# Kernel tuning notes

Measured on AMD Instinct MI355X. Metric: run time of the kernel, lower is better.

The kernel has to match this reference:

```python
import jax, jax.numpy as jnp
import numpy as np

BN_EPS = 1e-5


def setup_inputs() -> dict:
    key = jax.random.key(0)
    ks = jax.random.split(key, 8)
    B, C, H, W = 8, 256, 64, 64
    Ci = 128
    x = jax.random.normal(ks[0], (B, C, H, W), dtype=jnp.float32)
    # 1x1 conv weights stored as [out, in] (kernel size 1 squeezed)
    sc = 1.0 / np.sqrt(C)
    g_w = jax.random.uniform(ks[1], (Ci, C), jnp.float32, -sc, sc)
    g_b = jax.random.uniform(ks[2], (Ci,), jnp.float32, -sc, sc)
    theta_w = jax.random.uniform(ks[3], (Ci, C), jnp.float32, -sc, sc)
    theta_b = jax.random.uniform(ks[4], (Ci,), jnp.float32, -sc, sc)
    phi_w = jax.random.uniform(ks[5], (Ci, C), jnp.float32, -sc, sc)
    phi_b = jax.random.uniform(ks[6], (Ci,), jnp.float32, -sc, sc)
    # W conv: normal(std=0.01) weight, zero bias (per _init_weights)
    W_w = 0.01 * jax.random.normal(ks[7], (C, Ci), dtype=jnp.float32)
    W_b = jnp.zeros((C,), dtype=jnp.float32)
    bn_gamma = jnp.ones((C,), dtype=jnp.float32)
    bn_beta = jnp.zeros((C,), dtype=jnp.float32)
    return {"x": x, "g_w": g_w, "g_b": g_b, "theta_w": theta_w, "theta_b": theta_b,
            "phi_w": phi_w, "phi_b": phi_b, "W_w": W_w, "W_b": W_b,
            "bn_gamma": bn_gamma, "bn_beta": bn_beta}


def reference(x, g_w, g_b, theta_w, theta_b, phi_w, phi_b, W_w, W_b, bn_gamma, bn_beta):
    B, C, H, W = x.shape
    xf = x.reshape(B, C, H * W)                                   # [B, C, N]
    # 1x1 convs == per-position channel GEMMs
    g_x = jnp.einsum('oc,bcn->bon', g_w, xf) + g_b[:, None]        # [B, Ci, N]
    th = jnp.einsum('oc,bcn->bon', theta_w, xf) + theta_b[:, None]
    ph = jnp.einsum('oc,bcn->bon', phi_w, xf) + phi_b[:, None]
    # theta^T phi : [B, N, N] dense attention scores
    f = jnp.einsum('bcn,bcm->bnm', th, ph)
    attn = jax.nn.softmax(f, axis=-1)
    # attention-weighted sum of g values -> [B, Ci, N]
    y = jnp.einsum('bnm,bcm->bcn', attn, g_x)
    # output 1x1 conv + BatchNorm2d (training-mode batch stats)
    wy = jnp.einsum('oc,bcn->bon', W_w, y) + W_b[:, None]          # [B, C, N]
    mean = jnp.mean(wy, axis=(0, 2), keepdims=True)
    var = jnp.var(wy, axis=(0, 2), keepdims=True)
    wy_bn = (wy - mean) * jax.lax.rsqrt(var + BN_EPS)
    wy_bn = wy_bn * bn_gamma[:, None] + bn_beta[:, None]
    z = wy_bn.reshape(B, C, H, W) + x
    return z
```

## Files before the change

### kernel.cpp

```cpp
#include <hip/hip_runtime.h>
#include <math.h>

#define B_   8
#define C_   256
#define CI_  128
#define N_   4096

typedef unsigned short ushort_t;
typedef unsigned int uint_t;
typedef __attribute__((ext_vector_type(8))) short short8;
typedef __attribute__((ext_vector_type(16))) float floatx16;

#define OFF_W3B  0ull
#define OFF_B3   196608ull
#define OFF_XT   198144ull
#define OFF_THT  16975360ull
#define OFF_PHT  25363968ull
#define OFF_G16  33752576ull
#define OFF_LP   42141184ull
#define OFF_YP   42403328ull
#define OFF_YT   75957760ull
#define OFF_WY   198144ull
#define OFF_ST   92735232ull

__device__ __forceinline__ ushort_t f2bf(float x) {
  union { float f; uint_t u; } c; c.f = x;
  return (ushort_t)((c.u + 0x7fffu + ((c.u >> 16) & 1u)) >> 16);
}
__device__ __forceinline__ uint_t pack_bf2(float a, float b) {
  union { float f; uint_t u; } x, y; x.f = a; y.f = b;
  uint_t lo = (x.u + 0x7fffu + ((x.u >> 16) & 1u)) >> 16;
  uint_t hi = (y.u + 0x7fffu + ((y.u >> 16) & 1u)) & 0xffff0000u;
  return lo | hi;
}
__device__ __forceinline__ void async_copy16(const void* g, void* l) {
  __builtin_amdgcn_global_load_lds(
      (const __attribute__((address_space(1))) unsigned int*)g,
      (__attribute__((address_space(3))) unsigned int*)l, 16, 0, 0);
}

__global__ __launch_bounds__(256) void pack_w(
    const float* __restrict__ g_w, const float* __restrict__ g_b,
    const float* __restrict__ th_w, const float* __restrict__ th_b,
    const float* __restrict__ ph_w, const float* __restrict__ ph_b,
    ushort_t* __restrict__ W3b, float* __restrict__ b3)
{
  int i = blockIdx.x * 256 + threadIdx.x;
  int o = i >> 8;
  float v;
  if (o < 128)      v = g_w[i];
  else if (o < 256) v = th_w[i - 128*256];
  else              v = ph_w[i - 256*256];
  W3b[i] = f2bf(v);
  if ((i & 255) == 0)
    b3[o] = (o < 128) ? g_b[o] : (o < 256) ? th_b[o - 128] : ph_b[o - 256];
}

__global__ __launch_bounds__(256) void xcast(
    const float* __restrict__ x, ushort_t* __restrict__ xt)
{
  const int b = blockIdx.z, c0 = blockIdx.y * 64, n0 = blockIdx.x * 64;
  const int tid = threadIdx.x;
  __shared__ float xs[64][65];
  const int nq = (tid & 15) * 4, cr = tid >> 4;
  #pragma unroll
  for (int i = 0; i < 4; ++i) {
    float4 v = *(const float4*)&x[((size_t)b * C_ + c0 + cr + 16*i) * N_ + n0 + nq];
    xs[cr + 16*i][nq] = v.x; xs[cr + 16*i][nq+1] = v.y;
    xs[cr + 16*i][nq+2] = v.z; xs[cr + 16*i][nq+3] = v.w;
  }
  __syncthreads();
  const int n = tid >> 2, cs = (tid & 3) * 16;
  uint_t u[8];
  #pragma unroll
  for (int j = 0; j < 8; ++j)
    u[j] = pack_bf2(xs[cs + 2*j][n], xs[cs + 2*j + 1][n]);
  ushort_t* dst = &xt[((size_t)b * N_ + n0 + n) * C_ + c0 + cs];
  *(uint4*)dst       = make_uint4(u[0], u[1], u[2], u[3]);
  *(uint4*)(dst + 8) = make_uint4(u[4], u[5], u[6], u[7]);
}

template<int GMODE>
__global__ __launch_bounds__(256, 2) void proj_mfma(
    const ushort_t* __restrict__ W3b, const float* __restrict__ b3,
    const ushort_t* __restrict__ xt, ushort_t* __restrict__ tht,
    ushort_t* __restrict__ pht, ushort_t* __restrict__ g16)
{
  const int b = blockIdx.z, nb = blockIdx.x, ot = blockIdx.y;
  const int o0 = GMODE ? 0 : (128 + ot * 128);
  const int tid = threadIdx.x, w = tid >> 6, lane = tid & 63;
  const int l31 = lane & 31, h = lane >> 5, xk = l31 & 7;
  __shared__ ushort_t ws_l[128 * 64];
  __shared__ ushort_t xs_l[128 * 64];
  const ushort_t* xb = xt + (size_t)b * N_ * C_;
  const int n0 = nb * 128;
  floatx16 acc[4];
  #pragma unroll
  for (int ct = 0; ct < 4; ++ct)
    #pragma unroll
    for (int r = 0; r < 16; ++r) acc[ct][r] = 0.f;

  const int gr = lane >> 3, gu = lane & 7;
  for (int k0 = 0; k0 < C_; k0 += 64) {
    __syncthreads();
    #pragma unroll
    for (int i = 0; i < 4; ++i) {
      int r = w*32 + i*8 + gr;
      async_copy16(&W3b[(size_t)(o0 + r) * C_ + k0 + ((gu ^ (r & 7)) * 8)],
                   &ws_l[(w*32 + i*8) * 64]);
      async_copy16(&xb[(size_t)(n0 + r) * C_ + k0 + ((gu ^ (r & 7)) * 8)],
                   &xs_l[(w*32 + i*8) * 64]);
    }
    __syncthreads();
    #pragma unroll
    for (int kk = 0; kk < 4; ++kk) {
      int fc = ((2*kk + h) ^ xk) * 8;
      short8 bf = GMODE ? *(const short8*)&ws_l[(w*32 + l31) * 64 + fc]
                        : *(const short8*)&xs_l[(w*32 + l31) * 64 + fc];
      #pragma unroll
      for (int ct = 0; ct < 4; ++ct) {
        short8 af = GMODE ? *(const short8*)&xs_l[(ct*32 + l31) * 64 + fc]
                          : *(const short8*)&ws_l[(ct*32 + l31) * 64 + fc];
        acc[ct] = __builtin_amdgcn_mfma_f32_32x32x16_bf16(af, bf, acc[ct], 0, 0, 0);
      }
    }
  }

  if (GMODE) {
    float bv = b3[w*32 + l31];
    ushort_t* gp = g16 + ((size_t)b * CI_ + w*32 + l31) * N_;
    #pragma unroll
    for (int ct = 0; ct < 4; ++ct)
      #pragma unroll
      for (int rq = 0; rq < 4; ++rq) {
        uint2 d = make_uint2(pack_bf2(acc[ct][4*rq+0] + bv, acc[ct][4*rq+1] + bv),
                             pack_bf2(acc[ct][4*rq+2] + bv, acc[ct][4*rq+3] + bv));
        *(uint2*)&gp[n0 + ct*32 + 8*rq + 4*h] = d;
      }
  } else {
    ushort_t* tp = ((ot == 0) ? tht : pht) + ((size_t)b * N_ + n0 + w*32 + l31) * CI_;
    #pragma unroll
    for (int ct = 0; ct < 4; ++ct)
      #pragma unroll
      for (int rq = 0; rq < 4; ++rq) {
        float4 bv = *(const float4*)&b3[o0 + ct*32 + 8*rq + 4*h];
        uint2 d = make_uint2(pack_bf2(acc[ct][4*rq+0] + bv.x, acc[ct][4*rq+1] + bv.y),
                             pack_bf2(acc[ct][4*rq+2] + bv.z, acc[ct][4*rq+3] + bv.w));
        *(uint2*)&tp[ct*32 + 8*rq + 4*h] = d;
      }
  }
}

#define LOG2E_  1.442695041f
#define MBIAS_  (-28.85390082f)

__global__ __launch_bounds__(256, 2) void attn_mfma(
    const ushort_t* __restrict__ tht, const ushort_t* __restrict__ pht,
    const ushort_t* __restrict__ g16, float* __restrict__ yp,
    float* __restrict__ lp)
{
  const int b  = blockIdx.x & 7;
  const int ms = (blockIdx.x >> 3) & 1;
  const int qb = blockIdx.x >> 4;
  const int tid = threadIdx.x, w = tid >> 6, lane = tid & 63;
  const int l31 = lane & 31, h = lane >> 5, xk = l31 & 7;

  __shared__ ushort_t phs[64 * 128];
  __shared__ ushort_t gs [128 * 64];
  __shared__ ushort_t Pl [4][32 * 64];

  const int q0w = qb * 128 + w * 32;
  const int m_base = ms * 2048;

  const ushort_t* thb = tht + (size_t)b * N_ * CI_;
  const ushort_t* phb = pht + (size_t)b * N_ * CI_;
  const ushort_t* gbp = g16 + (size_t)b * CI_ * N_;

  short8 tf[8];
  #pragma unroll
  for (int kk = 0; kk < 8; ++kk)
    tf[kk] = *(const short8*)&thb[(size_t)(q0w + l31) * CI_ + kk*16 + h*8];

  floatx16 acc[4];
  #pragma unroll
  for (int ct = 0; ct < 4; ++ct)
    #pragma unroll
    for (int r = 0; r < 16; ++r) acc[ct][r] = 0.f;
  float lpart = 0.f;

  const int phr = lane >> 4, phu = lane & 15;
  const int gr  = lane >> 3, gu  = lane & 7;

  for (int m0 = m_base; m0 < m_base + 2048; m0 += 64) {
    __syncthreads();
    #pragma unroll
    for (int i = 0; i < 4; ++i) {
      int row = w*16 + i*4 + phr;
      async_copy16(&phb[(size_t)(m0 + row) * CI_ + ((phu ^ (row & 7)) * 8)],
                   &phs[(w*16 + i*4) * 128]);
    }
    #pragma unroll
    for (int i = 0; i < 4; ++i) {
      int c = w*32 + i*8 + gr;
      async_copy16(&gbp[(size_t)c * N_ + m0 + ((gu ^ (c & 7)) * 8)],
                   &gs[(w*32 + i*8) * 64]);
    }
    __syncthreads();

    #pragma unroll
    for (int mt = 0; mt < 2; ++mt) {
      floatx16 s;
      #pragma unroll
      for (int r = 0; r < 16; ++r) s[r] = 0.f;
      #pragma unroll
      for (int kk = 0; kk < 8; ++kk) {
        short8 pf = *(const short8*)&phs[(mt*32 + l31) * 128 + (((2*kk + h) ^ xk) * 8)];
        s = __builtin_amdgcn_mfma_f32_32x32x16_bf16(pf, tf[kk], s, 0, 0, 0);
      }
      float ls = 0.f;
      #pragma unroll
      for (int rq = 0; rq < 4; ++rq) {
        float p0 = exp2f(fmaf(s[4*rq+0], LOG2E_, MBIAS_));
        float p1 = exp2f(fmaf(s[4*rq+1], LOG2E_, MBIAS_));
        float p2 = exp2f(fmaf(s[4*rq+2], LOG2E_, MBIAS_));
        float p3 = exp2f(fmaf(s[4*rq+3], LOG2E_, MBIAS_));
        ls += (p0 + p1) + (p2 + p3);
        uint2 d = make_uint2(pack_bf2(p0, p1), pack_bf2(p2, p3));
        *(uint2*)&Pl[w][l31 * 64 + (((mt*4 + rq) ^ xk) * 8) + h*4] = d;
      }
      lpart += ls;
    }

    #pragma unroll
    for (int kk = 0; kk < 4; ++kk) {
      int pc = ((2*kk + h) ^ xk) * 8;
      short8 pfr = *(const short8*)&Pl[w][l31 * 64 + pc];
      #pragma unroll
      for (int ct = 0; ct < 4; ++ct) {
        short8 gf = *(const short8*)&gs[(ct*32 + l31) * 64 + pc];
        acc[ct] = __builtin_amdgcn_mfma_f32_32x32x16_bf16(gf, pfr, acc[ct], 0, 0, 0);
      }
    }
  }

  float lq = lpart + __shfl_xor(lpart, 32);
  if (h == 0)
    lp[((size_t)ms * 8 + b) * N_ + q0w + l31] = lq;
  float* ypb = yp + ((size_t)ms * 8 + b) * CI_ * N_;
  #pragma unroll
  for (int ct = 0; ct < 4; ++ct)
    #pragma unroll
    for (int r = 0; r < 16; ++r) {
      int c = ct*32 + (r & 3) + 8*(r >> 2) + 4*h;
      ypb[(size_t)c * N_ + q0w + l31] = acc[ct][r];
    }
}

__global__ __launch_bounds__(256) void combine(
    const float* __restrict__ yp, const float* __restrict__ lp,
    float* __restrict__ yt)
{
  size_t i = ((size_t)blockIdx.x * 256 + threadIdx.x) * 4;
  int q = (int)(i & 4095);
  int b = (int)(i >> 19);
  const size_t half = (size_t)8 * CI_ * N_;
  float4 y0 = *(const float4*)&yp[i];
  float4 y1 = *(const float4*)&yp[half + i];
  float4 l0 = *(const float4*)&lp[(size_t)b * N_ + q];
  float4 l1 = *(const float4*)&lp[(size_t)8 * N_ + (size_t)b * N_ + q];
  float4 o;
  o.x = (y0.x + y1.x) / (l0.x + l1.x);
  o.y = (y0.y + y1.y) / (l0.y + l1.y);
  o.z = (y0.z + y1.z) / (l0.z + l1.z);
  o.w = (y0.w + y1.w) / (l0.w + l1.w);
  *(float4*)&yt[i] = o;
}

__global__ __launch_bounds__(256) void gemm_bias(
    const float* __restrict__ A, const float* __restrict__ bias,
    const float* __restrict__ X, float* __restrict__ Out,
    int Odim, int Kdim)
{
  const int b  = blockIdx.z;
  const int o0 = blockIdx.y * 64;
  const int n0 = blockIdx.x * 64;
  const int tid = threadIdx.x;
  __shared__ float As[16 * 68];
  __shared__ float Xs[16 * 68];
  const int ty = tid >> 4, tx = tid & 15;
  float acc[4][4] = {};
  const float* Xb = X + (size_t)b * Kdim * N_;
  const int lkA = tid & 15, loA = tid >> 4;
  const int lnX = tid & 63, lkX = tid >> 6;

  for (int k0 = 0; k0 < Kdim; k0 += 16) {
    #pragma unroll
    for (int r = 0; r < 4; ++r)
      As[lkA * 68 + loA + 16 * r] = A[(size_t)(o0 + loA + 16 * r) * Kdim + k0 + lkA];
    #pragma unroll
    for (int r = 0; r < 4; ++r)
      Xs[(lkX + 4 * r) * 68 + lnX] = Xb[(size_t)(k0 + lkX + 4 * r) * N_ + n0 + lnX];
    __syncthreads();
    #pragma unroll
    for (int k = 0; k < 16; ++k) {
      float4 a4 = *(const float4*)&As[k * 68 + ty * 4];
      float4 x4 = *(const float4*)&Xs[k * 68 + tx * 4];
      float av[4] = {a4.x, a4.y, a4.z, a4.w};
      float xv[4] = {x4.x, x4.y, x4.z, x4.w};
      #pragma unroll
      for (int i = 0; i < 4; ++i)
        #pragma unroll
        for (int j = 0; j < 4; ++j)
          acc[i][j] += av[i] * xv[j];
    }
    __syncthreads();
  }
  #pragma unroll
  for (int i = 0; i < 4; ++i) {
    int o = o0 + ty * 4 + i;
    float bv = bias[o];
    float4 v = make_float4(acc[i][0] + bv, acc[i][1] + bv, acc[i][2] + bv, acc[i][3] + bv);
    *(float4*)&Out[((size_t)b * Odim + o) * N_ + n0 + tx * 4] = v;
  }
}

__global__ __launch_bounds__(256) void bn_stats(
    const float* __restrict__ WY, float* __restrict__ st)
{
  const int o = blockIdx.x;
  const int tid = threadIdx.x;
  float s = 0.f, s2 = 0.f;
  for (int b = 0; b < B_; ++b) {
    const float* p = WY + ((size_t)b * C_ + o) * N_;
    for (int n = tid * 4; n < N_; n += 256 * 4) {
      float4 v = *(const float4*)&p[n];
      s  += v.x + v.y + v.z + v.w;
      s2 += v.x * v.x + v.y * v.y + v.z * v.z + v.w * v.w;
    }
  }
  __shared__ float rs[256], rs2[256];
  rs[tid] = s; rs2[tid] = s2;
  __syncthreads();
  for (int off = 128; off > 0; off >>= 1) {
    if (tid < off) { rs[tid] += rs[tid + off]; rs2[tid] += rs2[tid + off]; }
    __syncthreads();
  }
  if (tid == 0) {
    const float M = (float)(B_ * N_);
    float mean = rs[0] / M;
    float var  = rs2[0] / M - mean * mean;
    st[o] = mean;
    st[256 + o] = rsqrtf(var + 1e-5f);
  }
}

__global__ __launch_bounds__(256) void bn_apply(
    const float* __restrict__ WY, const float* __restrict__ x,
    const float* __restrict__ st, const float* __restrict__ gamma,
    const float* __restrict__ beta, float* __restrict__ out)
{
  size_t i = ((size_t)blockIdx.x * 256 + threadIdx.x) * 4;
  int o = (int)((i >> 12) & 255);
  float4 w  = *(const float4*)&WY[i];
  float4 xv = *(const float4*)&x[i];
  float gsc = gamma[o] * st[256 + o];
  float bb  = beta[o] - st[o] * gsc;
  float4 v;
  v.x = w.x * gsc + bb + xv.x;
  v.y = w.y * gsc + bb + xv.y;
  v.z = w.z * gsc + bb + xv.z;
  v.w = w.w * gsc + bb + xv.w;
  *(float4*)&out[i] = v;
}

extern "C" void kernel_launch(void* const* d_in, const int* in_sizes, int n_in,
                              void* d_out, int out_size, void* d_ws, size_t ws_size,
                              hipStream_t stream)
{
  const float* x       = (const float*)d_in[0];
  const float* g_w     = (const float*)d_in[1];
  const float* g_b     = (const float*)d_in[2];
  const float* theta_w = (const float*)d_in[3];
  const float* theta_b = (const float*)d_in[4];
  const float* phi_w   = (const float*)d_in[5];
  const float* phi_b   = (const float*)d_in[6];
  const float* W_w     = (const float*)d_in[7];
  const float* W_b     = (const float*)d_in[8];
  const float* gamma   = (const float*)d_in[9];
  const float* beta    = (const float*)d_in[10];
  float* out = (float*)d_out;

  char* ws = (char*)d_ws;
  ushort_t* W3b = (ushort_t*)(ws + OFF_W3B);
  float*    b3  = (float*)(ws + OFF_B3);
  ushort_t* xt  = (ushort_t*)(ws + OFF_XT);
  ushort_t* tht = (ushort_t*)(ws + OFF_THT);
  ushort_t* pht = (ushort_t*)(ws + OFF_PHT);
  ushort_t* g16 = (ushort_t*)(ws + OFF_G16);
  float*    lpp = (float*)(ws + OFF_LP);
  float*    ypp = (float*)(ws + OFF_YP);
  float*    yt  = (float*)(ws + OFF_YT);
  float*    WY  = (float*)(ws + OFF_WY);
  float*    ST  = (float*)(ws + OFF_ST);

  pack_w<<<384, 256, 0, stream>>>(g_w, g_b, theta_w, theta_b, phi_w, phi_b, W3b, b3);
  xcast<<<dim3(64, 4, 8), 256, 0, stream>>>(x, xt);
  proj_mfma<0><<<dim3(32, 2, 8), 256, 0, stream>>>(W3b, b3, xt, tht, pht, g16);
  proj_mfma<1><<<dim3(32, 1, 8), 256, 0, stream>>>(W3b, b3, xt, tht, pht, g16);
  attn_mfma<<<512, 256, 0, stream>>>(tht, pht, g16, ypp, lpp);
  combine<<<4096, 256, 0, stream>>>(ypp, lpp, yt);
  gemm_bias<<<dim3(64, 4, 8), 256, 0, stream>>>(W_w, W_b, yt, WY, C_, CI_);
  bn_stats<<<256, 256, 0, stream>>>(WY, ST);
  bn_apply<<<8192, 256, 0, stream>>>(WY, x, ST, gamma, beta, out);
}
```

Before: 282.0 us.

## Double-buffer attention tiles, widen per-wave queries, bf16 intermediates, MFMA output GEMM

The attention kernel now gives each wave 64 queries (two 32-row tiles) so every staged phi/g tile is reused twice. It double-buffers the async LDS loads so the next tile loads while the current one is computed, and it writes partial outputs as bf16 in query-major layout through an LDS transpose. The combine step now reads and writes bf16, and the scalar fp32 output 1x1 conv is replaced with a bf16 MFMA GEMM using pre-packed weights. This is meant to cut memory traffic and scalar FMA cost, at the price of more registers, lower occupancy, half as many attention blocks, and extra bf16 rounding in y and in W.

```diff
diff --git a/kernel.cpp b/kernel.cpp
--- a/kernel.cpp
+++ b/kernel.cpp
@@ -13,15 +13,16 @@
 
 #define OFF_W3B  0ull
 #define OFF_B3   196608ull
-#define OFF_XT   198144ull
-#define OFF_THT  16975360ull
-#define OFF_PHT  25363968ull
-#define OFF_G16  33752576ull
-#define OFF_LP   42141184ull
-#define OFF_YP   42403328ull
-#define OFF_YT   75957760ull
-#define OFF_WY   198144ull
-#define OFF_ST   92735232ull
+#define OFF_WCB  198144ull
+#define OFF_XT   263680ull
+#define OFF_THT  17040896ull
+#define OFF_PHT  25429504ull
+#define OFF_G16  33818112ull
+#define OFF_LP   42206720ull
+#define OFF_YPB  42468864ull
+#define OFF_YTB  59246080ull
+#define OFF_WY   263680ull
+#define OFF_ST   67634688ull
 
 __device__ __forceinline__ ushort_t f2bf(float x) {
   union { float f; uint_t u; } c; c.f = x;
@@ -32,6 +33,12 @@
   uint_t lo = (x.u + 0x7fffu + ((x.u >> 16) & 1u)) >> 16;
   uint_t hi = (y.u + 0x7fffu + ((y.u >> 16) & 1u)) & 0xffff0000u;
   return lo | hi;
+}
+__device__ __forceinline__ float bf_lo(uint_t u) {
+  union { uint_t u; float f; } c; c.u = u << 16; return c.f;
+}
+__device__ __forceinline__ float bf_hi(uint_t u) {
+  union { uint_t u; float f; } c; c.u = u & 0xffff0000u; return c.f;
 }
 __device__ __forceinline__ void async_copy16(const void* g, void* l) {
   __builtin_amdgcn_global_load_lds(
@@ -56,6 +63,13 @@
     b3[o] = (o < 128) ? g_b[o] : (o < 256) ? th_b[o - 128] : ph_b[o - 256];
 }
 
+__global__ __launch_bounds__(256) void wpack(
+    const float* __restrict__ W_w, ushort_t* __restrict__ Wc)
+{
+  int i = blockIdx.x * 256 + threadIdx.x;
+  Wc[i] = f2bf(W_w[i]);
+}
+
 __global__ __launch_bounds__(256) void xcast(
     const float* __restrict__ x, ushort_t* __restrict__ xt)
 {
@@ -154,9 +168,9 @@
 #define LOG2E_  1.442695041f
 #define MBIAS_  (-28.85390082f)
 
-__global__ __launch_bounds__(256, 2) void attn_mfma(
+__global__ __launch_bounds__(256, 1) void attn_mfma(
     const ushort_t* __restrict__ tht, const ushort_t* __restrict__ pht,
-    const ushort_t* __restrict__ g16, float* __restrict__ yp,
+    const ushort_t* __restrict__ g16, ushort_t* __restrict__ yp,
     float* __restrict__ lp)
 {
   const int b  = blockIdx.x & 7;
@@ -165,163 +179,210 @@
   const int tid = threadIdx.x, w = tid >> 6, lane = tid & 63;
   const int l31 = lane & 31, h = lane >> 5, xk = l31 & 7;
 
-  __shared__ ushort_t phs[64 * 128];
-  __shared__ ushort_t gs [128 * 64];
-  __shared__ ushort_t Pl [4][32 * 64];
-
-  const int q0w = qb * 128 + w * 32;
+  __shared__ ushort_t smem[49152];
+
+  const int q0w = qb * 256 + w * 64;
   const int m_base = ms * 2048;
 
   const ushort_t* thb = tht + (size_t)b * N_ * CI_;
   const ushort_t* phb = pht + (size_t)b * N_ * CI_;
   const ushort_t* gbp = g16 + (size_t)b * CI_ * N_;
 
-  short8 tf[8];
-  #pragma unroll
-  for (int kk = 0; kk < 8; ++kk)
-    tf[kk] = *(const short8*)&thb[(size_t)(q0w + l31) * CI_ + kk*16 + h*8];
-
-  floatx16 acc[4];
-  #pragma unroll
-  for (int ct = 0; ct < 4; ++ct)
-    #pragma unroll
-    for (int r = 0; r < 16; ++r) acc[ct][r] = 0.f;
-  float lpart = 0.f;
-
-  const int phr = lane >> 4, phu = lane & 15;
-  const int gr  = lane >> 3, gu  = lane & 7;
-
-  for (int m0 = m_base; m0 < m_base + 2048; m0 += 64) {
-    __syncthreads();
+  short8 tf[2][8];
+  #pragma unroll
+  for (int qt = 0; qt < 2; ++qt)
+    #pragma unroll
+    for (int kk = 0; kk < 8; ++kk)
+      tf[qt][kk] = *(const short8*)&thb[(size_t)(q0w + qt*32 + l31) * CI_ + kk*16 + h*8];
+
+  floatx16 acc[2][4];
+  #pragma unroll
+  for (int qt = 0; qt < 2; ++qt)
+    #pragma unroll
+    for (int ct = 0; ct < 4; ++ct)
+      #pragma unroll
+      for (int r = 0; r < 16; ++r) acc[qt][ct][r] = 0.f;
+  float lpart[2] = {0.f, 0.f};
+
+  const int pRow = lane >> 4, pCol = lane & 15;
+  const int gRow = lane >> 3, gCol = lane & 7;
+
+  auto stage = [&](int m0, int buf) {
+    ushort_t* phd = smem + buf * 8192;
+    ushort_t* gd  = smem + 16384 + buf * 8192;
     #pragma unroll
     for (int i = 0; i < 4; ++i) {
-      int row = w*16 + i*4 + phr;
-      async_copy16(&phb[(size_t)(m0 + row) * CI_ + ((phu ^ (row & 7)) * 8)],
-                   &phs[(w*16 + i*4) * 128]);
+      int rb = i*16 + w*4;
+      int row = rb + pRow;
+      async_copy16(&phb[(size_t)(m0 + row) * CI_ + ((pCol ^ (row & 7)) * 8)],
+                   phd + rb * 128);
     }
     #pragma unroll
     for (int i = 0; i < 4; ++i) {
-      int c = w*32 + i*8 + gr;
-      async_copy16(&gbp[(size_t)c * N_ + m0 + ((gu ^ (c & 7)) * 8)],
-                   &gs[(w*32 + i*8) * 64]);
-    }
-    __syncthreads();
+      int rb = i*32 + w*8;
+      int row = rb + gRow;
+      async_copy16(&gbp[(size_t)row * N_ + m0 + ((gCol ^ (row & 7)) * 8)],
+                   gd + rb * 64);
+    }
+  };
+
+  stage(m_base, 0);
+
+  for (int it = 0; it < 32; ++it) {
+    const int buf = it & 1;
+    __syncthreads();
+    if (it + 1 < 32) stage(m_base + (it + 1) * 64, buf ^ 1);
+
+    const ushort_t* phs = smem + buf * 8192;
+    const ushort_t* gs  = smem + 16384 + buf * 8192;
+    ushort_t* Pl0 = smem + 32768 + (w*2 + 0) * 2048;
+    ushort_t* Pl1 = smem + 32768 + (w*2 + 1) * 2048;
 
     #pragma unroll
     for (int mt = 0; mt < 2; ++mt) {
-      floatx16 s;
-      #pragma unroll
-      for (int r = 0; r < 16; ++r) s[r] = 0.f;
+      floatx16 s0, s1;
+      #pragma unroll
+      for (int r = 0; r < 16; ++r) { s0[r] = 0.f; s1[r] = 0.f; }
       #pragma unroll
       for (int kk = 0; kk < 8; ++kk) {
         short8 pf = *(const short8*)&phs[(mt*32 + l31) * 128 + (((2*kk + h) ^ xk) * 8)];
-        s = __builtin_amdgcn_mfma_f32_32x32x16_bf16(pf, tf[kk], s, 0, 0, 0);
-      }
-      float ls = 0.f;
-      #pragma unroll
-      for (int rq = 0; rq < 4; ++rq) {
-        float p0 = exp2f(fmaf(s[4*rq+0], LOG2E_, MBIAS_));
-        float p1 = exp2f(fmaf(s[4*rq+1], LOG2E_, MBIAS_));
-        float p2 = exp2f(fmaf(s[4*rq+2], LOG2E_, MBIAS_));
-        float p3 = exp2f(fmaf(s[4*rq+3], LOG2E_, MBIAS_));
-        ls += (p0 + p1) + (p2 + p3);
-        uint2 d = make_uint2(pack_bf2(p0, p1), pack_bf2(p2, p3));
-        *(uint2*)&Pl[w][l31 * 64 + (((mt*4 + rq) ^ xk) * 8) + h*4] = d;
-      }
-      lpart += ls;
+        s0 = __builtin_amdgcn_mfma_f32_32x32x16_bf16(pf, tf[0][kk], s0, 0, 0, 0);
+        s1 = __builtin_amdgcn_mfma_f32_32x32x16_bf16(pf, tf[1][kk], s1, 0, 0, 0);
+      }
+      #pragma unroll
+      for (int qt = 0; qt < 2; ++qt) {
+        const floatx16& s = qt ? s1 : s0;
+        ushort_t* Pq = qt ? Pl1 : Pl0;
+        float ls = 0.f;
+        #pragma unroll
+        for (int rq = 0; rq < 4; ++rq) {
+          float p0 = exp2f(fmaf(s[4*rq+0], LOG2E_, MBIAS_));
+          float p1 = exp2f(fmaf(s[4*rq+1], LOG2E_, MBIAS_));
+          float p2 = exp2f(fmaf(s[4*rq+2], LOG2E_, MBIAS_));
+          float p3 = exp2f(fmaf(s[4*rq+3], LOG2E_, MBIAS_));
+          ls += (p0 + p1) + (p2 + p3);
+          uint2 d = make_uint2(pack_bf2(p0, p1), pack_bf2(p2, p3));
+          *(uint2*)&Pq[l31 * 64 + (((mt*4 + rq) ^ xk) * 8) + h*4] = d;
+        }
+        lpart[qt] += ls;
+      }
     }
 
     #pragma unroll
     for (int kk = 0; kk < 4; ++kk) {
       int pc = ((2*kk + h) ^ xk) * 8;
-      short8 pfr = *(const short8*)&Pl[w][l31 * 64 + pc];
+      short8 p0 = *(const short8*)&Pl0[l31 * 64 + pc];
+      short8 p1 = *(const short8*)&Pl1[l31 * 64 + pc];
       #pragma unroll
       for (int ct = 0; ct < 4; ++ct) {
         short8 gf = *(const short8*)&gs[(ct*32 + l31) * 64 + pc];
-        acc[ct] = __builtin_amdgcn_mfma_f32_32x32x16_bf16(gf, pfr, acc[ct], 0, 0, 0);
-      }
-    }
-  }
-
-  float lq = lpart + __shfl_xor(lpart, 32);
-  if (h == 0)
-    lp[((size_t)ms * 8 + b) * N_ + q0w + l31] = lq;
-  float* ypb = yp + ((size_t)ms * 8 + b) * CI_ * N_;
+        acc[0][ct] = __builtin_amdgcn_mfma_f32_32x32x16_bf16(gf, p0, acc[0][ct], 0, 0, 0);
+        acc[1][ct] = __builtin_amdgcn_mfma_f32_32x32x16_bf16(gf, p1, acc[1][ct], 0, 0, 0);
+      }
+    }
+  }
+
+  #pragma unroll
+  for (int qt = 0; qt < 2; ++qt) {
+    float lq = lpart[qt] + __shfl_xor(lpart[qt], 32);
+    if (h == 0)
+      lp[((size_t)ms * 8 + b) * N_ + q0w + qt*32 + l31] = lq;
+  }
+
+  __syncthreads();
+  ushort_t* tr = smem + w * 8192;
+  #pragma unroll
+  for (int qt = 0; qt < 2; ++qt)
+    #pragma unroll
+    for (int ct = 0; ct < 4; ++ct)
+      #pragma unroll
+      for (int rq = 0; rq < 4; ++rq) {
+        uint2 d = make_uint2(pack_bf2(acc[qt][ct][4*rq+0], acc[qt][ct][4*rq+1]),
+                             pack_bf2(acc[qt][ct][4*rq+2], acc[qt][ct][4*rq+3]));
+        *(uint2*)&tr[(qt*32 + l31) * 128 + ct*32 + 8*rq + 4*h] = d;
+      }
+  ushort_t* ypb = yp + (((size_t)ms * 8 + b) * N_ + q0w) * CI_;
+  #pragma unroll
+  for (int itx = 0; itx < 16; ++itx) {
+    int row = itx*4 + (lane >> 4);
+    int cu  = (lane & 15) * 8;
+    uint4 v = *(const uint4*)&tr[row * 128 + cu];
+    *(uint4*)&ypb[(size_t)row * CI_ + cu] = v;
+  }
+}
+
+__global__ __launch_bounds__(256) void combine(
+    const ushort_t* __restrict__ yp, const float* __restrict__ lp,
+    ushort_t* __restrict__ ytb)
+{
+  size_t idx = (size_t)blockIdx.x * 256 + threadIdx.x;
+  size_t i = idx * 8;
+  int q_lin = (int)(i >> 7);
+  const size_t halfU = (size_t)B_ * N_ * CI_ / 8;
+  uint4 a = ((const uint4*)yp)[idx];
+  uint4 c = ((const uint4*)yp)[halfU + idx];
+  float inv = 1.0f / (lp[q_lin] + lp[(size_t)B_ * N_ + q_lin]);
+  uint4 o;
+  o.x = pack_bf2((bf_lo(a.x) + bf_lo(c.x)) * inv, (bf_hi(a.x) + bf_hi(c.x)) * inv);
+  o.y = pack_bf2((bf_lo(a.y) + bf_lo(c.y)) * inv, (bf_hi(a.y) + bf_hi(c.y)) * inv);
+  o.z = pack_bf2((bf_lo(a.z) + bf_lo(c.z)) * inv, (bf_hi(a.z) + bf_hi(c.z)) * inv);
+  o.w = pack_bf2((bf_lo(a.w) + bf_lo(c.w)) * inv, (bf_hi(a.w) + bf_hi(c.w)) * inv);
+  ((uint4*)ytb)[idx] = o;
+}
+
+__global__ __launch_bounds__(256, 2) void wgemm_mfma(
+    const ushort_t* __restrict__ Wc, const float* __restrict__ Wb,
+    const ushort_t* __restrict__ ytb, float* __restrict__ WY)
+{
+  const int b = blockIdx.z, nb = blockIdx.x, ot = blockIdx.y;
+  const int o0 = ot * 128;
+  const int tid = threadIdx.x, w = tid >> 6, lane = tid & 63;
+  const int l31 = lane & 31, h = lane >> 5, xk = l31 & 7;
+  __shared__ ushort_t ws_l[128 * 64];
+  __shared__ ushort_t xs_l[128 * 64];
+  const ushort_t* xb = ytb + (size_t)b * N_ * CI_;
+  const int n0 = nb * 128;
+  floatx16 acc[4];
   #pragma unroll
   for (int ct = 0; ct < 4; ++ct)
     #pragma unroll
-    for (int r = 0; r < 16; ++r) {
-      int c = ct*32 + (r & 3) + 8*(r >> 2) + 4*h;
-      ypb[(size_t)c * N_ + q0w + l31] = acc[ct][r];
-    }
-}
-
-__global__ __launch_bounds__(256) void combine(
-    const float* __restrict__ yp, const float* __restrict__ lp,
-    float* __restrict__ yt)
-{
-  size_t i = ((size_t)blockIdx.x * 256 + threadIdx.x) * 4;
-  int q = (int)(i & 4095);
-  int b = (int)(i >> 19);
-  const size_t half = (size_t)8 * CI_ * N_;
-  float4 y0 = *(const float4*)&yp[i];
-  float4 y1 = *(const float4*)&yp[half + i];
-  float4 l0 = *(const float4*)&lp[(size_t)b * N_ + q];
-  float4 l1 = *(const float4*)&lp[(size_t)8 * N_ + (size_t)b * N_ + q];
-  float4 o;
-  o.x = (y0.x + y1.x) / (l0.x + l1.x);
-  o.y = (y0.y + y1.y) / (l0.y + l1.y);
-  o.z = (y0.z + y1.z) / (l0.z + l1.z);
-  o.w = (y0.w + y1.w) / (l0.w + l1.w);
-  *(float4*)&yt[i] = o;
-}
-
-__global__ __launch_bounds__(256) void gemm_bias(
-    const float* __restrict__ A, const float* __restrict__ bias,
-    const float* __restrict__ X, float* __restrict__ Out,
-    int Odim, int Kdim)
-{
-  const int b  = blockIdx.z;
-  const int o0 = blockIdx.y * 64;
-  const int n0 = blockIdx.x * 64;
-  const int tid = threadIdx.x;
-  __shared__ float As[16 * 68];
-  __shared__ float Xs[16 * 68];
-  const int ty = tid >> 4, tx = tid & 15;
-  float acc[4][4] = {};
-  const float* Xb = X + (size_t)b * Kdim * N_;
-  const int lkA = tid & 15, loA = tid >> 4;
-  const int lnX = tid & 63, lkX = tid >> 6;
-
-  for (int k0 = 0; k0 < Kdim; k0 += 16) {
-    #pragma unroll
-    for (int r = 0; r < 4; ++r)
-      As[lkA * 68 + loA + 16 * r] = A[(size_t)(o0 + loA + 16 * r) * Kdim + k0 + lkA];
-    #pragma unroll
-    for (int r = 0; r < 4; ++r)
-      Xs[(lkX + 4 * r) * 68 + lnX] = Xb[(size_t)(k0 + lkX + 4 * r) * N_ + n0 + lnX];
-    __syncthreads();
-    #pragma unroll
-    for (int k = 0; k < 16; ++k) {
-      float4 a4 = *(const float4*)&As[k * 68 + ty * 4];
-      float4 x4 = *(const float4*)&Xs[k * 68 + tx * 4];
-      float av[4] = {a4.x, a4.y, a4.z, a4.w};
-      float xv[4] = {x4.x, x4.y, x4.z, x4.w};
-      #pragma unroll
-      for (int i = 0; i < 4; ++i)
-        #pragma unroll
-        for (int j = 0; j < 4; ++j)
-          acc[i][j] += av[i] * xv[j];
-    }
-    __syncthreads();
-  }
-  #pragma unroll
-  for (int i = 0; i < 4; ++i) {
-    int o = o0 + ty * 4 + i;
-    float bv = bias[o];
-    float4 v = make_float4(acc[i][0] + bv, acc[i][1] + bv, acc[i][2] + bv, acc[i][3] + bv);
-    *(float4*)&Out[((size_t)b * Odim + o) * N_ + n0 + tx * 4] = v;
-  }
+    for (int r = 0; r < 16; ++r) acc[ct][r] = 0.f;
+
+  const int gr = lane >> 3, gu = lane & 7;
+  for (int k0 = 0; k0 < CI_; k0 += 64) {
+    __syncthreads();
+    #pragma unroll
+    for (int i = 0; i < 4; ++i) {
+      int r = w*32 + i*8 + gr;
+      async_copy16(&Wc[(size_t)(o0 + r) * CI_ + k0 + ((gu ^ (r & 7)) * 8)],
+                   &ws_l[(w*32 + i*8) * 64]);
+      async_copy16(&xb[(size_t)(n0 + r) * CI_ + k0 + ((gu ^ (r & 7)) * 8)],
+                   &xs_l[(w*32 + i*8) * 64]);
+    }
+    __syncthreads();
+    #pragma unroll
+    for (int kk = 0; kk < 4; ++kk) {
+      int fc = ((2*kk + h) ^ xk) * 8;
+      short8 bf = *(const short8*)&xs_l[(w*32 + l31) * 64 + fc];
+      #pragma unroll
+      for (int ct = 0; ct < 4; ++ct) {
+        short8 af = *(const short8*)&ws_l[(ct*32 + l31) * 64 + fc];
+        acc[ct] = __builtin_amdgcn_mfma_f32_32x32x16_bf16(af, bf, acc[ct], 0, 0, 0);
+      }
+    }
+  }
+  const int n = n0 + w*32 + l31;
+  #pragma unroll
+  for (int ct = 0; ct < 4; ++ct)
+    #pragma unroll
+    for (int rq = 0; rq < 4; ++rq) {
+      float4 bv = *(const float4*)&Wb[o0 + ct*32 + 8*rq + 4*h];
+      #pragma unroll
+      for (int j = 0; j < 4; ++j) {
+        int o = o0 + ct*32 + 8*rq + 4*h + j;
+        WY[((size_t)b * C_ + o) * N_ + n] = acc[ct][4*rq + j] + (&bv.x)[j];
+      }
+    }
 }
 
 __global__ __launch_bounds__(256) void bn_stats(
@@ -393,23 +454,25 @@
   char* ws = (char*)d_ws;
   ushort_t* W3b = (ushort_t*)(ws + OFF_W3B);
   float*    b3  = (float*)(ws + OFF_B3);
+  ushort_t* Wc  = (ushort_t*)(ws + OFF_WCB);
   ushort_t* xt  = (ushort_t*)(ws + OFF_XT);
   ushort_t* tht = (ushort_t*)(ws + OFF_THT);
   ushort_t* pht = (ushort_t*)(ws + OFF_PHT);
   ushort_t* g16 = (ushort_t*)(ws + OFF_G16);
   float*    lpp = (float*)(ws + OFF_LP);
-  float*    ypp = (float*)(ws + OFF_YP);
-  float*    yt  = (float*)(ws + OFF_YT);
+  ushort_t* ypb = (ushort_t*)(ws + OFF_YPB);
+  ushort_t* ytb = (ushort_t*)(ws + OFF_YTB);
   float*    WY  = (float*)(ws + OFF_WY);
   float*    ST  = (float*)(ws + OFF_ST);
 
   pack_w<<<384, 256, 0, stream>>>(g_w, g_b, theta_w, theta_b, phi_w, phi_b, W3b, b3);
+  wpack<<<128, 256, 0, stream>>>(W_w, Wc);
   xcast<<<dim3(64, 4, 8), 256, 0, stream>>>(x, xt);
   proj_mfma<0><<<dim3(32, 2, 8), 256, 0, stream>>>(W3b, b3, xt, tht, pht, g16);
   proj_mfma<1><<<dim3(32, 1, 8), 256, 0, stream>>>(W3b, b3, xt, tht, pht, g16);
-  attn_mfma<<<512, 256, 0, stream>>>(tht, pht, g16, ypp, lpp);
-  combine<<<4096, 256, 0, stream>>>(ypp, lpp, yt);
-  gemm_bias<<<dim3(64, 4, 8), 256, 0, stream>>>(W_w, W_b, yt, WY, C_, CI_);
+  attn_mfma<<<256, 256, 0, stream>>>(tht, pht, g16, ypb, lpp);
+  combine<<<2048, 256, 0, stream>>>(ypb, lpp, ytb);
+  wgemm_mfma<<<dim3(32, 2, 8), 256, 0, stream>>>(Wc, W_b, ytb, WY);
   bn_stats<<<256, 256, 0, stream>>>(WY, ST);
   bn_apply<<<8192, 256, 0, stream>>>(WY, x, ST, gamma, beta, out);
 }
```

After: 288.0 us. 2.1% more time.
